# Performance work log

Hardware: AMD Instinct MI355X
Metric: run time of the kernel (lower is better)

Reference implementation:

```python
import jax, jax.numpy as jnp
import numpy as np
from jax import lax

N = 100000          # nodes
C = 64              # classes
E = 1600000         # edges (avg degree 16)
EPS = 1e-8
PROP_STEPS = 3
ALPHA = 0.2
GLOBAL_BETA = 0.05
MIN_ANCHOR = 0.6
RESIDUAL_SCALE = 0.15
DEGREE_BIAS = 0.25
COHERENCE_BIAS = 0.2
CLUSTERING_BIAS = 0.2
GRAPH_SCALE_BIAS = 1.0
SRC_CENTER = 0.55
SRC_SHARP = 8.0
REC_CENTER = 0.5
REC_SHARP = 8.0
ACCEPT_SHARP = 12.0
ACCEPT_THRESH = 0.0
QW = 0.7   # accept_quality_weight
MW = 0.2   # accept_margin_weight
SW = 0.1   # accept_struct_weight
LOG_C = float(np.log(C))


def _spmm(edge_src, edge_dst, w, x):
    # sparse adj @ x : out[d] = sum_{e: dst(e)=d} w[e] * x[src(e)]
    return jax.ops.segment_sum(w[:, None] * x[edge_src], edge_dst, num_segments=N)


def _cos(a, b):
    # F.cosine_similarity(dim=1, eps=1e-8), keepdims
    na = jnp.maximum(jnp.linalg.norm(a, axis=1, keepdims=True), 1e-8)
    nb = jnp.maximum(jnp.linalg.norm(b, axis=1, keepdims=True), 1e-8)
    return jnp.sum(a * b, axis=1, keepdims=True) / (na * nb)


def _confidence(state):
    mass = jnp.sum(state, axis=1, keepdims=True)                 # [N,1]
    norm = state / (mass + EPS)
    entropy = -jnp.sum(norm * jnp.log(norm + EPS), axis=1, keepdims=True)
    certainty = 1.0 - entropy / LOG_C
    mass_scale = jnp.maximum(lax.stop_gradient(jnp.mean(mass)), EPS)
    magnitude = jnp.tanh(mass / mass_scale)
    return jnp.clip(0.5 * certainty + 0.5 * magnitude, 0.0, 1.0)


def _quality(state, ctx, clustering):
    lq = jnp.clip((_cos(state, ctx) + 1.0) * 0.5, 0.0, 1.0)
    probs = state / (jnp.sum(state, axis=1, keepdims=True) + EPS)
    top2, _ = lax.top_k(probs, 2)
    margin = top2[:, :1] - top2[:, 1:2]
    return QW * lq + MW * margin + SW * clustering


def _forward(logits, edge_weight, struct_feat, edge_src, edge_dst):
    seed = jax.nn.relu(logits)
    confidence = _confidence(seed)                                # [N,1]
    global_prior = jnp.sum(confidence * seed, axis=0, keepdims=True) / \
        jnp.maximum(jnp.sum(confidence), EPS)                     # [1,C]
    anchor = jnp.clip(MIN_ANCHOR + ALPHA * confidence, 0.0, 0.995)
    uncertainty = 1.0 - confidence
    log_degree = struct_feat[:, :1]
    low_degree = jnp.clip(1.0 - log_degree, 0.0, 1.0)
    clustering = struct_feat[:, 1:2]
    low_clustering = jnp.clip(1.0 - clustering, 0.0, 1.0)
    graph_scale = jnp.clip(1.0 - jnp.mean(clustering), 0.2, 1.0)
    # gates depend only on confidence -> identical every step
    source_gate = jax.nn.sigmoid(SRC_SHARP * (confidence - SRC_CENTER))
    recipient_gate = jax.nn.sigmoid(REC_SHARP * (REC_CENTER - confidence))

    propagated = seed
    for _ in range(PROP_STEPS):
        weighted_state = source_gate * propagated
        local_num = _spmm(edge_src, edge_dst, edge_weight, weighted_state)
        local_den = jnp.maximum(_spmm(edge_src, edge_dst, edge_weight, source_gate), EPS)
        local_context = local_num / local_den
        fused = (1.0 - GLOBAL_BETA) * local_context + GLOBAL_BETA * global_prior
        agreement = jnp.clip((_cos(propagated, fused) + 1.0) * 0.5, 0.0, 1.0)
        seed_agree = jnp.clip((_cos(seed, fused) + 1.0) * 0.5, 0.0, 1.0)
        sel = jnp.clip(uncertainty + DEGREE_BIAS * low_degree +
                       COHERENCE_BIAS * seed_agree + CLUSTERING_BIAS * low_clustering, 0.0, 1.0)
        update_gate = recipient_gate * sel * agreement * (1.0 - anchor)
        residual = RESIDUAL_SCALE * GRAPH_SCALE_BIAS * graph_scale * update_gate * (fused - propagated)
        propagated = jnp.maximum(anchor * seed + (1.0 - anchor) * propagated + residual, 0.0)

    base_ctx = _spmm(edge_src, edge_dst, edge_weight, seed)
    prop_ctx = _spmm(edge_src, edge_dst, edge_weight, propagated)
    base_q = _quality(seed, base_ctx, clustering)
    prop_q = _quality(propagated, prop_ctx, clustering)
    accept = jax.nn.sigmoid(ACCEPT_SHARP * (prop_q - base_q - ACCEPT_THRESH))
    return accept * propagated + (1.0 - accept) * seed


def setup_inputs() -> dict:
    key = jax.random.key(0)
    k1, k2, k3, k4, k5 = jax.random.split(key, 5)
    return {
        "logits": jax.random.normal(k1, (N, C), dtype=jnp.float32),
        "edge_weight": jax.random.uniform(k2, (E,), dtype=jnp.float32),
        "struct_feat": jax.random.uniform(k3, (N, 2), dtype=jnp.float32),
        "edge_src": jax.random.randint(k4, (E,), 0, N, dtype=jnp.int32),
        "edge_dst": jax.random.randint(k5, (E,), 0, N, dtype=jnp.int32),
    }


def reference(logits, edge_weight, struct_feat, edge_src, edge_dst):
    return _forward(logits, edge_weight, struct_feat, edge_src, edge_dst)
```

## Files before the change

### kernel.cpp

```cpp
#include <hip/hip_runtime.h>
#include <math.h>

#define NN 100000
#define CC 64
#define EPSF 1e-8f
#define LOG_C 4.1588830833596715f
#define SCAN_BS 1024
#define NSB ((NN + SCAN_BS - 1) / SCAN_BS)

__device__ __forceinline__ float waveSum(float v) {
#pragma unroll
    for (int off = 32; off; off >>= 1) v += __shfl_xor(v, off);
    return v;
}
__device__ __forceinline__ float redChanSum(float v) {
#pragma unroll
    for (int off = 8; off; off >>= 1) v += __shfl_xor(v, off);
    return v;
}
__device__ __forceinline__ float redChanMax(float v) {
#pragma unroll
    for (int off = 8; off; off >>= 1) v = fmaxf(v, __shfl_xor(v, off));
    return v;
}
__device__ __forceinline__ float redGrpSum(float v) {
    v += __shfl_xor(v, 16);
    v += __shfl_xor(v, 32);
    return v;
}
__device__ __forceinline__ float clip01(float v) { return fminf(fmaxf(v, 0.f), 1.f); }
__device__ __forceinline__ float sigmoidf(float x) { return 1.f / (1.f + expf(-x)); }


__global__ void k_seed(const float* __restrict__ logits, const float* __restrict__ sf,
                       float* __restrict__ seed, float* __restrict__ prop,
                       float* __restrict__ mass, float* __restrict__ cert,
                       float* __restrict__ scal) {
    int lane = threadIdx.x & 63;
    int wid = threadIdx.x >> 6;
    float accm = 0.f, accc = 0.f;
    for (int row = blockIdx.x * 4 + wid; row < NN; row += gridDim.x * 4) {
        float l = logits[row * CC + lane];
        float s = fmaxf(l, 0.f);
        seed[row * CC + lane] = s;
        prop[row * CC + lane] = s;
        float m = waveSum(s);
        float nrm = s / (m + EPSF);
        float ent = waveSum(-nrm * logf(nrm + EPSF));
        if (lane == 0) {
            mass[row] = m;
            cert[row] = 1.f - ent / LOG_C;
            accm += m;
            accc += sf[row * 2 + 1];
        }
    }
    __shared__ float sm[8];
    if (lane == 0) { sm[wid] = accm; sm[4 + wid] = accc; }
    __syncthreads();
    if (threadIdx.x == 0) {
        atomicAdd(&scal[0], sm[0] + sm[1] + sm[2] + sm[3]);
        atomicAdd(&scal[1], sm[4] + sm[5] + sm[6] + sm[7]);
    }
}

__global__ void k_conf(const float* __restrict__ seed, const float* __restrict__ mass,
                       const float* __restrict__ cert, float* __restrict__ conf,
                       float* __restrict__ sg, float* __restrict__ scal,
                       float* __restrict__ gp) {
    int lane = threadIdx.x & 63;
    int wid = threadIdx.x >> 6;
    float msc = fmaxf(scal[0] * (1.f / NN), EPSF);
    float accgp = 0.f, accconf = 0.f;
    for (int row = blockIdx.x * 4 + wid; row < NN; row += gridDim.x * 4) {
        float m = mass[row], ct = cert[row];
        float cf = clip01(0.5f * ct + 0.5f * tanhf(m / msc));
        accgp += cf * seed[row * CC + lane];
        if (lane == 0) {
            conf[row] = cf;
            sg[row] = sigmoidf(8.f * (cf - 0.55f));
            accconf += cf;
        }
    }
    __shared__ float sgp[256];
    __shared__ float scf[4];
    sgp[threadIdx.x] = accgp;
    if (lane == 0) scf[wid] = accconf;
    __syncthreads();
    if (threadIdx.x < 64)
        atomicAdd(&gp[lane], sgp[lane] + sgp[64 + lane] + sgp[128 + lane] + sgp[192 + lane]);
    if (threadIdx.x == 0) atomicAdd(&scal[2], scf[0] + scf[1] + scf[2] + scf[3]);
}

__global__ void k_finalize(float* __restrict__ scal, float* __restrict__ gp) {
    float sc = fmaxf(scal[2], EPSF);
    gp[threadIdx.x] = gp[threadIdx.x] / sc;
    if (threadIdx.x == 0) {
        scal[3] = fminf(fmaxf(1.f - scal[1] * (1.f / NN), 0.2f), 1.f);
    }
}


__global__ void k_hist(const int* __restrict__ dst, int* __restrict__ count, int E) {
    int i = blockIdx.x * blockDim.x + threadIdx.x;
    int stride = gridDim.x * blockDim.x;
    for (; i < E; i += stride) atomicAdd(&count[dst[i]], 1);
}

__global__ void k_bsum(const int* __restrict__ count, int* __restrict__ bsum) {
    int b = blockIdx.x, t = threadIdx.x;
    int base = b * SCAN_BS + t * 4;
    int s = 0;
#pragma unroll
    for (int k = 0; k < 4; ++k) {
        int i = base + k;
        if (i < NN) s += count[i];
    }
#pragma unroll
    for (int off = 32; off; off >>= 1) s += __shfl_xor(s, off);
    __shared__ int red[4];
    if ((t & 63) == 0) red[t >> 6] = s;
    __syncthreads();
    if (t == 0) bsum[b] = red[0] + red[1] + red[2] + red[3];
}

__global__ void k_boff(const int* __restrict__ bsum, int* __restrict__ boff,
                       int* __restrict__ row_start) {
    int acc = 0;
    for (int i = 0; i < NSB; ++i) { boff[i] = acc; acc += bsum[i]; }
    row_start[NN] = acc;
}

__global__ void k_scanwrite(const int* __restrict__ count, const int* __restrict__ boff,
                            int* __restrict__ row_start, int* __restrict__ cursor) {
    int b = blockIdx.x, t = threadIdx.x, lane = t & 63, wid = t >> 6;
    int base = b * SCAN_BS + t * 4;
    int c0 = 0, c1 = 0, c2 = 0, c3 = 0;
    if (base < NN) c0 = count[base];
    if (base + 1 < NN) c1 = count[base + 1];
    if (base + 2 < NN) c2 = count[base + 2];
    if (base + 3 < NN) c3 = count[base + 3];
    int s = c0 + c1 + c2 + c3;
    int incl = s;
#pragma unroll
    for (int off = 1; off < 64; off <<= 1) {
        int o = __shfl_up(incl, off);
        if (lane >= off) incl += o;
    }
    __shared__ int wsum[4];
    if (lane == 63) wsum[wid] = incl;
    __syncthreads();
    int woff = 0;
    for (int i = 0; i < wid; ++i) woff += wsum[i];
    int excl = boff[b] + woff + incl - s;
    if (base < NN) { row_start[base] = excl; cursor[base] = excl; excl += c0; }
    if (base + 1 < NN) { row_start[base + 1] = excl; cursor[base + 1] = excl; excl += c1; }
    if (base + 2 < NN) { row_start[base + 2] = excl; cursor[base + 2] = excl; excl += c2; }
    if (base + 3 < NN) { row_start[base + 3] = excl; cursor[base + 3] = excl; excl += c3; }
}

__global__ void k_scatter(const int* __restrict__ src, const int* __restrict__ dst,
                          const float* __restrict__ w, int* __restrict__ cursor,
                          int2* __restrict__ edge_pk, int E) {
    int i = blockIdx.x * blockDim.x + threadIdx.x;
    int stride = gridDim.x * blockDim.x;
    for (; i < E; i += stride) {
        int d = dst[i];
        int pos = atomicAdd(&cursor[d], 1);
        edge_pk[pos] = make_int2(src[i], __float_as_int(w[i]));
    }
}


template <int MODE>
__global__ __launch_bounds__(256) void k_csr(
    const int2* __restrict__ edge_pk, const int* __restrict__ row_start,
    const float* __restrict__ x, const float* __restrict__ sg,
    const float* __restrict__ seed, const float* __restrict__ sf,
    float* __restrict__ den, float* __restrict__ bq,
    float* __restrict__ numo, const float* __restrict__ baseq,
    float* __restrict__ outp) {
    int lane = threadIdx.x & 63;
    int row = blockIdx.x * 4 + (threadIdx.x >> 6);
    if (row >= NN) return;
    int grp = lane >> 4, cidx = lane & 15;
    int rs = row_start[row], re = row_start[row + 1];

    float4 acc = make_float4(0.f, 0.f, 0.f, 0.f);
    float4 accn = make_float4(0.f, 0.f, 0.f, 0.f);
    float accden = 0.f;

    for (int base = rs; base < re; base += 8) {
        int e0 = base + grp;
        int e1 = base + 4 + grp;
        int2 pk0 = make_int2(0, 0), pk1 = make_int2(0, 0);
        if (e0 < re) pk0 = edge_pk[e0];
        if (e1 < re) pk1 = edge_pk[e1];
        float w0 = __int_as_float(pk0.y);
        float w1 = __int_as_float(pk1.y);
        const float4 xv0 = *(const float4*)(x + pk0.x * CC + cidx * 4);
        const float4 xv1 = *(const float4*)(x + pk1.x * CC + cidx * 4);
        if (MODE == 0) {
            float ws0 = w0 * sg[pk0.x];
            float ws1 = w1 * sg[pk1.x];
            acc.x += w0 * xv0.x + w1 * xv1.x;
            acc.y += w0 * xv0.y + w1 * xv1.y;
            acc.z += w0 * xv0.z + w1 * xv1.z;
            acc.w += w0 * xv0.w + w1 * xv1.w;
            accn.x += ws0 * xv0.x + ws1 * xv1.x;
            accn.y += ws0 * xv0.y + ws1 * xv1.y;
            accn.z += ws0 * xv0.z + ws1 * xv1.z;
            accn.w += ws0 * xv0.w + ws1 * xv1.w;
            accden += ws0 + ws1;
        } else if (MODE == 1) {
            float ws0 = w0 * sg[pk0.x];
            float ws1 = w1 * sg[pk1.x];
            acc.x += ws0 * xv0.x + ws1 * xv1.x;
            acc.y += ws0 * xv0.y + ws1 * xv1.y;
            acc.z += ws0 * xv0.z + ws1 * xv1.z;
            acc.w += ws0 * xv0.w + ws1 * xv1.w;
        } else {
            acc.x += w0 * xv0.x + w1 * xv1.x;
            acc.y += w0 * xv0.y + w1 * xv1.y;
            acc.z += w0 * xv0.z + w1 * xv1.z;
            acc.w += w0 * xv0.w + w1 * xv1.w;
        }
    }

    acc.x = redGrpSum(acc.x); acc.y = redGrpSum(acc.y);
    acc.z = redGrpSum(acc.z); acc.w = redGrpSum(acc.w);

    if (MODE == 1) {
        if (grp == 0) *(float4*)(numo + row * CC + cidx * 4) = acc;
        return;
    }

    const float4 s4 = *(const float4*)(((MODE == 0) ? seed : x) + row * CC + cidx * 4);
    float dot = s4.x * acc.x + s4.y * acc.y + s4.z * acc.z + s4.w * acc.w;
    float ss = s4.x * s4.x + s4.y * s4.y + s4.z * s4.z + s4.w * s4.w;
    float cc2 = acc.x * acc.x + acc.y * acc.y + acc.z * acc.z + acc.w * acc.w;
    float m = s4.x + s4.y + s4.z + s4.w;
    dot = redChanSum(dot);
    ss = redChanSum(ss);
    cc2 = redChanSum(cc2);
    m = redChanSum(m);
    float cosv = dot / (fmaxf(sqrtf(ss), 1e-8f) * fmaxf(sqrtf(cc2), 1e-8f));
    float lq = clip01((cosv + 1.f) * 0.5f);
    float inv = 1.f / (m + EPSF);
    float p0 = s4.x * inv, p1 = s4.y * inv, p2 = s4.z * inv, p3 = s4.w * inv;
    float m1 = redChanMax(fmaxf(fmaxf(p0, p1), fmaxf(p2, p3)));
    float cnt = (p0 == m1) + (p1 == m1) + (p2 == m1) + (p3 == m1);
    float mlt = -3.4e38f;
    mlt = fmaxf(mlt, (p0 < m1) ? p0 : -3.4e38f);
    mlt = fmaxf(mlt, (p1 < m1) ? p1 : -3.4e38f);
    mlt = fmaxf(mlt, (p2 < m1) ? p2 : -3.4e38f);
    mlt = fmaxf(mlt, (p3 < m1) ? p3 : -3.4e38f);
    cnt = redChanSum(cnt);
    mlt = redChanMax(mlt);
    float m2 = (cnt >= 2.f) ? m1 : mlt;
    float q = 0.7f * lq + 0.2f * (m1 - m2) + 0.1f * sf[row * 2 + 1];

    if (MODE == 0) {
        accn.x = redGrpSum(accn.x); accn.y = redGrpSum(accn.y);
        accn.z = redGrpSum(accn.z); accn.w = redGrpSum(accn.w);
        float dsum = accden;
        dsum += __shfl_xor(dsum, 16);
        dsum += __shfl_xor(dsum, 32);
        if (grp == 0) *(float4*)(numo + row * CC + cidx * 4) = accn;
        if (lane == 0) {
            den[row] = dsum;
            bq[row] = q;
        }
    } else {
        float accp = sigmoidf(12.f * (q - baseq[row]));
        const float4 sd = *(const float4*)(seed + row * CC + cidx * 4);
        if (grp == 0) {
            float4 o;
            o.x = accp * s4.x + (1.f - accp) * sd.x;
            o.y = accp * s4.y + (1.f - accp) * sd.y;
            o.z = accp * s4.z + (1.f - accp) * sd.z;
            o.w = accp * s4.w + (1.f - accp) * sd.w;
            *(float4*)(outp + row * CC + cidx * 4) = o;
        }
    }
}


__global__ __launch_bounds__(256) void k_update(
    const float* __restrict__ num, const float* __restrict__ den,
    const float* __restrict__ gp, const float* __restrict__ conf,
    const float* __restrict__ sf, const float* __restrict__ seed,
    float* __restrict__ prop, const float* __restrict__ scal) {
    int cidx = threadIdx.x & 15;
    int row = blockIdx.x * 16 + (threadIdx.x >> 4);
    if (row >= NN) return;
    float dn = fmaxf(den[row], EPSF);
    float inv = 1.f / dn;
    const float4 n4 = *(const float4*)(num + row * CC + cidx * 4);
    const float4 g4 = *(const float4*)(gp + cidx * 4);
    const float4 p4 = *(const float4*)(prop + row * CC + cidx * 4);
    const float4 s4 = *(const float4*)(seed + row * CC + cidx * 4);
    float4 f4;
    f4.x = 0.95f * (n4.x * inv) + 0.05f * g4.x;
    f4.y = 0.95f * (n4.y * inv) + 0.05f * g4.y;
    f4.z = 0.95f * (n4.z * inv) + 0.05f * g4.z;
    f4.w = 0.95f * (n4.w * inv) + 0.05f * g4.w;
    float pf = p4.x * f4.x + p4.y * f4.y + p4.z * f4.z + p4.w * f4.w;
    float pp = p4.x * p4.x + p4.y * p4.y + p4.z * p4.z + p4.w * p4.w;
    float ff = f4.x * f4.x + f4.y * f4.y + f4.z * f4.z + f4.w * f4.w;
    float sfv = s4.x * f4.x + s4.y * f4.y + s4.z * f4.z + s4.w * f4.w;
    float ss = s4.x * s4.x + s4.y * s4.y + s4.z * s4.z + s4.w * s4.w;
    pf = redChanSum(pf);
    pp = redChanSum(pp);
    ff = redChanSum(ff);
    sfv = redChanSum(sfv);
    ss = redChanSum(ss);
    float nf = fmaxf(sqrtf(ff), 1e-8f);
    float agree = clip01((pf / (fmaxf(sqrtf(pp), 1e-8f) * nf) + 1.f) * 0.5f);
    float sagree = clip01((sfv / (fmaxf(sqrtf(ss), 1e-8f) * nf) + 1.f) * 0.5f);
    float cf = conf[row];
    float anchor = fminf(fmaxf(0.6f + 0.2f * cf, 0.f), 0.995f);
    float unc = 1.f - cf;
    float lowdeg = clip01(1.f - sf[row * 2 + 0]);
    float lowcl = clip01(1.f - sf[row * 2 + 1]);
    float rec = sigmoidf(8.f * (0.5f - cf));
    float sel = clip01(unc + 0.25f * lowdeg + 0.2f * sagree + 0.2f * lowcl);
    float ug = rec * sel * agree * (1.f - anchor);
    float rsc = 0.15f * scal[3] * ug;
    float4 o;
    o.x = fmaxf(anchor * s4.x + (1.f - anchor) * p4.x + rsc * (f4.x - p4.x), 0.f);
    o.y = fmaxf(anchor * s4.y + (1.f - anchor) * p4.y + rsc * (f4.y - p4.y), 0.f);
    o.z = fmaxf(anchor * s4.z + (1.f - anchor) * p4.z + rsc * (f4.z - p4.z), 0.f);
    o.w = fmaxf(anchor * s4.w + (1.f - anchor) * p4.w + rsc * (f4.w - p4.w), 0.f);
    *(float4*)(prop + row * CC + cidx * 4) = o;
}


extern "C" void kernel_launch(void* const* d_in, const int* in_sizes, int n_in,
                              void* d_out, int out_size, void* d_ws, size_t ws_size,
                              hipStream_t stream) {
    const float* logits = (const float*)d_in[0];
    const float* ew = (const float*)d_in[1];
    const float* sf = (const float*)d_in[2];
    const int* esrc = (const int*)d_in[3];
    const int* edst = (const int*)d_in[4];
    float* out = (float*)d_out;
    int E = in_sizes[1];

    float* ws = (float*)d_ws;
    float* seed = ws;
    float* prop = seed + NN * CC;
    int2* edge_pk = (int2*)(prop + NN * CC);
    size_t foff = (size_t)2 * NN * CC + 2 * (size_t)E;
    foff = (foff + 3) & ~(size_t)3;
    float* fbase = ws + foff;
    float* massA = fbase;
    float* certA = massA + NN;
    float* confA = certA + NN;
    float* sgA = confA + NN;
    float* denA = sgA + NN;
    float* bqA = denA + NN;
    float* scal = bqA + NN;
    float* gp = scal + 8;
    int* count = (int*)(gp + 64);
    int* cursor = count + NN;
    int* row_start = cursor + NN;
    int* bsum = row_start + NN + 1;
    int* boff = bsum + NSB;
    float* num = out;

    hipMemsetAsync(scal, 0, (8 + 64) * sizeof(float), stream);
    hipMemsetAsync(count, 0, NN * sizeof(int), stream);

    const int redBlocks = 1024;
    const int rowBlocks = (NN + 3) / 4;
    const int rowBlocks16 = (NN + 15) / 16;
    const int edgeBlocks = 1024;

    k_seed<<<redBlocks, 256, 0, stream>>>(logits, sf, seed, prop, massA, certA, scal);
    k_conf<<<redBlocks, 256, 0, stream>>>(seed, massA, certA, confA, sgA, scal, gp);
    k_finalize<<<1, 64, 0, stream>>>(scal, gp);

    k_hist<<<edgeBlocks, 256, 0, stream>>>(edst, count, E);
    k_bsum<<<NSB, 256, 0, stream>>>(count, bsum);
    k_boff<<<1, 1, 0, stream>>>(bsum, boff, row_start);
    k_scanwrite<<<NSB, 256, 0, stream>>>(count, boff, row_start, cursor);
    k_scatter<<<edgeBlocks, 256, 0, stream>>>(esrc, edst, ew, cursor, edge_pk, E);

    k_csr<0><<<rowBlocks, 256, 0, stream>>>(edge_pk, row_start, seed, sgA, seed, sf,
                                            denA, bqA, num, nullptr, nullptr);
    k_update<<<rowBlocks16, 256, 0, stream>>>(num, denA, gp, confA, sf, seed, prop, scal);

    for (int t = 1; t < 3; ++t) {
        k_csr<1><<<rowBlocks, 256, 0, stream>>>(edge_pk, row_start, prop, sgA, seed, sf,
                                                nullptr, nullptr, num, nullptr, nullptr);
        k_update<<<rowBlocks16, 256, 0, stream>>>(num, denA, gp, confA, sf, seed, prop, scal);
    }

    k_csr<2><<<rowBlocks, 256, 0, stream>>>(edge_pk, row_start, prop, sgA, seed, sf,
                                            nullptr, nullptr, nullptr, bqA, out);
}
```

Before: 632.3 us.

## Fuse propagation update into CSR SpMM and two-level bin the edge scatter

Moves the per-row update (normalisation, agreement, anchor blend) into the CSR aggregation kernels and drops the separate k_update launches. The propagated state now ping-pongs between a workspace buffer and the output buffer instead of round-tripping a numerator array. Edge CSR construction becomes a two-pass scheme: edges are first binned by 64-row bucket, then each bucket is redistributed per row from LDS. This aims to reduce atomic contention and scattered writes. The src index is packed with the destination's low bits in 17 bits, which assumes fewer than 131072 nodes. Buckets with more than 4096 edges are silently truncated.

```diff
diff --git a/kernel.cpp b/kernel.cpp
--- a/kernel.cpp
+++ b/kernel.cpp
@@ -7,6 +7,8 @@
 #define LOG_C 4.1588830833596715f
 #define SCAN_BS 1024
 #define NSB ((NN + SCAN_BS - 1) / SCAN_BS)
+#define NB ((NN + 63) / 64)
+#define UNBIN_CAP 4096
 
 __device__ __forceinline__ float waveSum(float v) {
 #pragma unroll
@@ -33,9 +35,8 @@
 
 
 __global__ void k_seed(const float* __restrict__ logits, const float* __restrict__ sf,
-                       float* __restrict__ seed, float* __restrict__ prop,
-                       float* __restrict__ mass, float* __restrict__ cert,
-                       float* __restrict__ scal) {
+                       float* __restrict__ seed, float* __restrict__ mass,
+                       float* __restrict__ cert, float* __restrict__ scal) {
     int lane = threadIdx.x & 63;
     int wid = threadIdx.x >> 6;
     float accm = 0.f, accc = 0.f;
@@ -43,7 +44,6 @@
         float l = logits[row * CC + lane];
         float s = fmaxf(l, 0.f);
         seed[row * CC + lane] = s;
-        prop[row * CC + lane] = s;
         float m = waveSum(s);
         float nrm = s / (m + EPSF);
         float ent = waveSum(-nrm * logf(nrm + EPSF));
@@ -131,7 +131,8 @@
 }
 
 __global__ void k_scanwrite(const int* __restrict__ count, const int* __restrict__ boff,
-                            int* __restrict__ row_start, int* __restrict__ cursor) {
+                            int* __restrict__ row_start, int* __restrict__ cursor,
+                            int* __restrict__ bucket_cursor) {
     int b = blockIdx.x, t = threadIdx.x, lane = t & 63, wid = t >> 6;
     int base = b * SCAN_BS + t * 4;
     int c0 = 0, c1 = 0, c2 = 0, c3 = 0;
@@ -152,21 +153,44 @@
     int woff = 0;
     for (int i = 0; i < wid; ++i) woff += wsum[i];
     int excl = boff[b] + woff + incl - s;
+    if (((base & 63) == 0) && base < NN) bucket_cursor[base >> 6] = excl;
     if (base < NN) { row_start[base] = excl; cursor[base] = excl; excl += c0; }
     if (base + 1 < NN) { row_start[base + 1] = excl; cursor[base + 1] = excl; excl += c1; }
     if (base + 2 < NN) { row_start[base + 2] = excl; cursor[base + 2] = excl; excl += c2; }
     if (base + 3 < NN) { row_start[base + 3] = excl; cursor[base + 3] = excl; excl += c3; }
 }
 
-__global__ void k_scatter(const int* __restrict__ src, const int* __restrict__ dst,
-                          const float* __restrict__ w, int* __restrict__ cursor,
-                          int2* __restrict__ edge_pk, int E) {
+__global__ void k_binscatter(const int* __restrict__ src, const int* __restrict__ dst,
+                             const float* __restrict__ w, int* __restrict__ bucket_cursor,
+                             int2* __restrict__ edge_pk, int E) {
     int i = blockIdx.x * blockDim.x + threadIdx.x;
     int stride = gridDim.x * blockDim.x;
     for (; i < E; i += stride) {
         int d = dst[i];
+        int b = d >> 6;
+        int pos = atomicAdd(&bucket_cursor[b], 1);
+        edge_pk[pos] = make_int2(src[i] | ((d & 63) << 17), __float_as_int(w[i]));
+    }
+}
+
+__global__ __launch_bounds__(256) void k_unbin(const int* __restrict__ row_start,
+                                               int* __restrict__ cursor,
+                                               int2* __restrict__ edge_pk) {
+    __shared__ int2 buf[UNBIN_CAP];
+    int b = blockIdx.x;
+    int r0 = b << 6;
+    int bs = row_start[r0];
+    int r1 = min(r0 + 64, NN);
+    int be = row_start[r1];
+    int sz = min(be - bs, UNBIN_CAP);
+    for (int i = threadIdx.x; i < sz; i += 256) buf[i] = edge_pk[bs + i];
+    __syncthreads();
+    for (int i = threadIdx.x; i < sz; i += 256) {
+        int2 t = buf[i];
+        int srcv = t.x & 0x1FFFF;
+        int d = r0 + ((t.x >> 17) & 63);
         int pos = atomicAdd(&cursor[d], 1);
-        edge_pk[pos] = make_int2(src[i], __float_as_int(w[i]));
+        edge_pk[pos] = make_int2(srcv, t.y);
     }
 }
 
@@ -176,9 +200,9 @@
     const int2* __restrict__ edge_pk, const int* __restrict__ row_start,
     const float* __restrict__ x, const float* __restrict__ sg,
     const float* __restrict__ seed, const float* __restrict__ sf,
-    float* __restrict__ den, float* __restrict__ bq,
-    float* __restrict__ numo, const float* __restrict__ baseq,
-    float* __restrict__ outp) {
+    const float* __restrict__ conf, const float* __restrict__ gp,
+    const float* __restrict__ scal, float* __restrict__ den,
+    float* __restrict__ bq, float* __restrict__ pout) {
     int lane = threadIdx.x & 63;
     int row = blockIdx.x * 4 + (threadIdx.x >> 6);
     if (row >= NN) return;
@@ -230,7 +254,45 @@
     acc.z = redGrpSum(acc.z); acc.w = redGrpSum(acc.w);
 
     if (MODE == 1) {
-        if (grp == 0) *(float4*)(numo + row * CC + cidx * 4) = acc;
+        float dn = fmaxf(den[row], EPSF);
+        float inv = 1.f / dn;
+        const float4 g4 = *(const float4*)(gp + cidx * 4);
+        float4 f4;
+        f4.x = 0.95f * (acc.x * inv) + 0.05f * g4.x;
+        f4.y = 0.95f * (acc.y * inv) + 0.05f * g4.y;
+        f4.z = 0.95f * (acc.z * inv) + 0.05f * g4.z;
+        f4.w = 0.95f * (acc.w * inv) + 0.05f * g4.w;
+        const float4 p4 = *(const float4*)(x + row * CC + cidx * 4);
+        const float4 s4 = *(const float4*)(seed + row * CC + cidx * 4);
+        float pf = p4.x * f4.x + p4.y * f4.y + p4.z * f4.z + p4.w * f4.w;
+        float pp = p4.x * p4.x + p4.y * p4.y + p4.z * p4.z + p4.w * p4.w;
+        float ff = f4.x * f4.x + f4.y * f4.y + f4.z * f4.z + f4.w * f4.w;
+        float sfv = s4.x * f4.x + s4.y * f4.y + s4.z * f4.z + s4.w * f4.w;
+        float ss = s4.x * s4.x + s4.y * s4.y + s4.z * s4.z + s4.w * s4.w;
+        pf = redChanSum(pf);
+        pp = redChanSum(pp);
+        ff = redChanSum(ff);
+        sfv = redChanSum(sfv);
+        ss = redChanSum(ss);
+        float nf = fmaxf(sqrtf(ff), 1e-8f);
+        float agree = clip01((pf / (fmaxf(sqrtf(pp), 1e-8f) * nf) + 1.f) * 0.5f);
+        float sagree = clip01((sfv / (fmaxf(sqrtf(ss), 1e-8f) * nf) + 1.f) * 0.5f);
+        float cf = conf[row];
+        float anchor = fminf(fmaxf(0.6f + 0.2f * cf, 0.f), 0.995f);
+        float lowdeg = clip01(1.f - sf[row * 2 + 0]);
+        float lowcl = clip01(1.f - sf[row * 2 + 1]);
+        float rec = sigmoidf(8.f * (0.5f - cf));
+        float sel = clip01((1.f - cf) + 0.25f * lowdeg + 0.2f * sagree + 0.2f * lowcl);
+        float ug = rec * sel * agree * (1.f - anchor);
+        float rsc = 0.15f * scal[3] * ug;
+        if (grp == 0) {
+            float4 o;
+            o.x = fmaxf(anchor * s4.x + (1.f - anchor) * p4.x + rsc * (f4.x - p4.x), 0.f);
+            o.y = fmaxf(anchor * s4.y + (1.f - anchor) * p4.y + rsc * (f4.y - p4.y), 0.f);
+            o.z = fmaxf(anchor * s4.z + (1.f - anchor) * p4.z + rsc * (f4.z - p4.z), 0.f);
+            o.w = fmaxf(anchor * s4.w + (1.f - anchor) * p4.w + rsc * (f4.w - p4.w), 0.f);
+            *(float4*)(pout + row * CC + cidx * 4) = o;
+        }
         return;
     }
 
@@ -245,8 +307,8 @@
     m = redChanSum(m);
     float cosv = dot / (fmaxf(sqrtf(ss), 1e-8f) * fmaxf(sqrtf(cc2), 1e-8f));
     float lq = clip01((cosv + 1.f) * 0.5f);
-    float inv = 1.f / (m + EPSF);
-    float p0 = s4.x * inv, p1 = s4.y * inv, p2 = s4.z * inv, p3 = s4.w * inv;
+    float minv = 1.f / (m + EPSF);
+    float p0 = s4.x * minv, p1 = s4.y * minv, p2 = s4.z * minv, p3 = s4.w * minv;
     float m1 = redChanMax(fmaxf(fmaxf(p0, p1), fmaxf(p2, p3)));
     float cnt = (p0 == m1) + (p1 == m1) + (p2 == m1) + (p3 == m1);
     float mlt = -3.4e38f;
@@ -265,13 +327,42 @@
         float dsum = accden;
         dsum += __shfl_xor(dsum, 16);
         dsum += __shfl_xor(dsum, 32);
-        if (grp == 0) *(float4*)(numo + row * CC + cidx * 4) = accn;
+        float dn = fmaxf(dsum, EPSF);
+        float inv = 1.f / dn;
+        const float4 g4 = *(const float4*)(gp + cidx * 4);
+        float4 f4;
+        f4.x = 0.95f * (accn.x * inv) + 0.05f * g4.x;
+        f4.y = 0.95f * (accn.y * inv) + 0.05f * g4.y;
+        f4.z = 0.95f * (accn.z * inv) + 0.05f * g4.z;
+        f4.w = 0.95f * (accn.w * inv) + 0.05f * g4.w;
+        float sfv = s4.x * f4.x + s4.y * f4.y + s4.z * f4.z + s4.w * f4.w;
+        float ff = f4.x * f4.x + f4.y * f4.y + f4.z * f4.z + f4.w * f4.w;
+        sfv = redChanSum(sfv);
+        ff = redChanSum(ff);
+        float nf = fmaxf(sqrtf(ff), 1e-8f);
+        float sagree = clip01((sfv / (fmaxf(sqrtf(ss), 1e-8f) * nf) + 1.f) * 0.5f);
+        float cf = conf[row];
+        float anchor = fminf(fmaxf(0.6f + 0.2f * cf, 0.f), 0.995f);
+        float lowdeg = clip01(1.f - sf[row * 2 + 0]);
+        float lowcl = clip01(1.f - sf[row * 2 + 1]);
+        float rec = sigmoidf(8.f * (0.5f - cf));
+        float sel = clip01((1.f - cf) + 0.25f * lowdeg + 0.2f * sagree + 0.2f * lowcl);
+        float ug = rec * sel * sagree * (1.f - anchor);
+        float rsc = 0.15f * scal[3] * ug;
+        if (grp == 0) {
+            float4 o;
+            o.x = fmaxf(s4.x + rsc * (f4.x - s4.x), 0.f);
+            o.y = fmaxf(s4.y + rsc * (f4.y - s4.y), 0.f);
+            o.z = fmaxf(s4.z + rsc * (f4.z - s4.z), 0.f);
+            o.w = fmaxf(s4.w + rsc * (f4.w - s4.w), 0.f);
+            *(float4*)(pout + row * CC + cidx * 4) = o;
+        }
         if (lane == 0) {
             den[row] = dsum;
             bq[row] = q;
         }
     } else {
-        float accp = sigmoidf(12.f * (q - baseq[row]));
+        float accp = sigmoidf(12.f * (q - bq[row]));
         const float4 sd = *(const float4*)(seed + row * CC + cidx * 4);
         if (grp == 0) {
             float4 o;
@@ -279,59 +370,9 @@
             o.y = accp * s4.y + (1.f - accp) * sd.y;
             o.z = accp * s4.z + (1.f - accp) * sd.z;
             o.w = accp * s4.w + (1.f - accp) * sd.w;
-            *(float4*)(outp + row * CC + cidx * 4) = o;
-        }
-    }
-}
-
-
-__global__ __launch_bounds__(256) void k_update(
-    const float* __restrict__ num, const float* __restrict__ den,
-    const float* __restrict__ gp, const float* __restrict__ conf,
-    const float* __restrict__ sf, const float* __restrict__ seed,
-    float* __restrict__ prop, const float* __restrict__ scal) {
-    int cidx = threadIdx.x & 15;
-    int row = blockIdx.x * 16 + (threadIdx.x >> 4);
-    if (row >= NN) return;
-    float dn = fmaxf(den[row], EPSF);
-    float inv = 1.f / dn;
-    const float4 n4 = *(const float4*)(num + row * CC + cidx * 4);
-    const float4 g4 = *(const float4*)(gp + cidx * 4);
-    const float4 p4 = *(const float4*)(prop + row * CC + cidx * 4);
-    const float4 s4 = *(const float4*)(seed + row * CC + cidx * 4);
-    float4 f4;
-    f4.x = 0.95f * (n4.x * inv) + 0.05f * g4.x;
-    f4.y = 0.95f * (n4.y * inv) + 0.05f * g4.y;
-    f4.z = 0.95f * (n4.z * inv) + 0.05f * g4.z;
-    f4.w = 0.95f * (n4.w * inv) + 0.05f * g4.w;
-    float pf = p4.x * f4.x + p4.y * f4.y + p4.z * f4.z + p4.w * f4.w;
-    float pp = p4.x * p4.x + p4.y * p4.y + p4.z * p4.z + p4.w * p4.w;
-    float ff = f4.x * f4.x + f4.y * f4.y + f4.z * f4.z + f4.w * f4.w;
-    float sfv = s4.x * f4.x + s4.y * f4.y + s4.z * f4.z + s4.w * f4.w;
-    float ss = s4.x * s4.x + s4.y * s4.y + s4.z * s4.z + s4.w * s4.w;
-    pf = redChanSum(pf);
-    pp = redChanSum(pp);
-    ff = redChanSum(ff);
-    sfv = redChanSum(sfv);
-    ss = redChanSum(ss);
-    float nf = fmaxf(sqrtf(ff), 1e-8f);
-    float agree = clip01((pf / (fmaxf(sqrtf(pp), 1e-8f) * nf) + 1.f) * 0.5f);
-    float sagree = clip01((sfv / (fmaxf(sqrtf(ss), 1e-8f) * nf) + 1.f) * 0.5f);
-    float cf = conf[row];
-    float anchor = fminf(fmaxf(0.6f + 0.2f * cf, 0.f), 0.995f);
-    float unc = 1.f - cf;
-    float lowdeg = clip01(1.f - sf[row * 2 + 0]);
-    float lowcl = clip01(1.f - sf[row * 2 + 1]);
-    float rec = sigmoidf(8.f * (0.5f - cf));
-    float sel = clip01(unc + 0.25f * lowdeg + 0.2f * sagree + 0.2f * lowcl);
-    float ug = rec * sel * agree * (1.f - anchor);
-    float rsc = 0.15f * scal[3] * ug;
-    float4 o;
-    o.x = fmaxf(anchor * s4.x + (1.f - anchor) * p4.x + rsc * (f4.x - p4.x), 0.f);
-    o.y = fmaxf(anchor * s4.y + (1.f - anchor) * p4.y + rsc * (f4.y - p4.y), 0.f);
-    o.z = fmaxf(anchor * s4.z + (1.f - anchor) * p4.z + rsc * (f4.z - p4.z), 0.f);
-    o.w = fmaxf(anchor * s4.w + (1.f - anchor) * p4.w + rsc * (f4.w - p4.w), 0.f);
-    *(float4*)(prop + row * CC + cidx * 4) = o;
+            *(float4*)(pout + row * CC + cidx * 4) = o;
+        }
+    }
 }
 
 
@@ -348,54 +389,49 @@
 
     float* ws = (float*)d_ws;
     float* seed = ws;
-    float* prop = seed + NN * CC;
-    int2* edge_pk = (int2*)(prop + NN * CC);
-    size_t foff = (size_t)2 * NN * CC + 2 * (size_t)E;
-    foff = (foff + 3) & ~(size_t)3;
-    float* fbase = ws + foff;
-    float* massA = fbase;
+    float* propA = seed + NN * CC;
+    int2* edge_pk = (int2*)(propA + NN * CC);
+    float* fb = (float*)(edge_pk + E);
+    float* massA = fb;
     float* certA = massA + NN;
     float* confA = certA + NN;
     float* sgA = confA + NN;
     float* denA = sgA + NN;
     float* bqA = denA + NN;
     float* scal = bqA + NN;
-    float* gp = scal + 8;
+    float* gp = scal + 16;
     int* count = (int*)(gp + 64);
     int* cursor = count + NN;
     int* row_start = cursor + NN;
     int* bsum = row_start + NN + 1;
     int* boff = bsum + NSB;
-    float* num = out;
-
-    hipMemsetAsync(scal, 0, (8 + 64) * sizeof(float), stream);
+    int* bucket_cursor = boff + NSB;
+    float* propB = out;
+
+    hipMemsetAsync(scal, 0, 16 * sizeof(float), stream);
     hipMemsetAsync(count, 0, NN * sizeof(int), stream);
 
     const int redBlocks = 1024;
     const int rowBlocks = (NN + 3) / 4;
-    const int rowBlocks16 = (NN + 15) / 16;
     const int edgeBlocks = 1024;
 
-    k_seed<<<redBlocks, 256, 0, stream>>>(logits, sf, seed, prop, massA, certA, scal);
+    k_seed<<<redBlocks, 256, 0, stream>>>(logits, sf, seed, massA, certA, scal);
     k_conf<<<redBlocks, 256, 0, stream>>>(seed, massA, certA, confA, sgA, scal, gp);
     k_finalize<<<1, 64, 0, stream>>>(scal, gp);
 
     k_hist<<<edgeBlocks, 256, 0, stream>>>(edst, count, E);
     k_bsum<<<NSB, 256, 0, stream>>>(count, bsum);
     k_boff<<<1, 1, 0, stream>>>(bsum, boff, row_start);
-    k_scanwrite<<<NSB, 256, 0, stream>>>(count, boff, row_start, cursor);
-    k_scatter<<<edgeBlocks, 256, 0, stream>>>(esrc, edst, ew, cursor, edge_pk, E);
+    k_scanwrite<<<NSB, 256, 0, stream>>>(count, boff, row_start, cursor, bucket_cursor);
+    k_binscatter<<<edgeBlocks, 256, 0, stream>>>(esrc, edst, ew, bucket_cursor, edge_pk, E);
+    k_unbin<<<NB, 256, 0, stream>>>(row_start, cursor, edge_pk);
 
     k_csr<0><<<rowBlocks, 256, 0, stream>>>(edge_pk, row_start, seed, sgA, seed, sf,
-                                            denA, bqA, num, nullptr, nullptr);
-    k_update<<<rowBlocks16, 256, 0, stream>>>(num, denA, gp, confA, sf, seed, prop, scal);
-
-    for (int t = 1; t < 3; ++t) {
-        k_csr<1><<<rowBlocks, 256, 0, stream>>>(edge_pk, row_start, prop, sgA, seed, sf,
-                                                nullptr, nullptr, num, nullptr, nullptr);
-        k_update<<<rowBlocks16, 256, 0, stream>>>(num, denA, gp, confA, sf, seed, prop, scal);
-    }
-
-    k_csr<2><<<rowBlocks, 256, 0, stream>>>(edge_pk, row_start, prop, sgA, seed, sf,
-                                            nullptr, nullptr, nullptr, bqA, out);
-}
+                                            confA, gp, scal, denA, bqA, propA);
+    k_csr<1><<<rowBlocks, 256, 0, stream>>>(edge_pk, row_start, propA, sgA, seed, sf,
+                                            confA, gp, scal, denA, bqA, propB);
+    k_csr<1><<<rowBlocks, 256, 0, stream>>>(edge_pk, row_start, propB, sgA, seed, sf,
+                                            confA, gp, scal, denA, bqA, propA);
+    k_csr<2><<<rowBlocks, 256, 0, stream>>>(edge_pk, row_start, propA, sgA, seed, sf,
+                                            confA, gp, scal, denA, bqA, out);
+}
```

Result: slower. 766.2 us (+21.2%).
